# Performance work log

Measured on AMD Instinct MI355X. Metric: run time of the kernel, lower is better.

## Reference

```python
import jax, jax.numpy as jnp
import numpy as np

N = 100000
E = 1600000
NFEAT = 128
NHID1 = 128
NHID2 = 128
NCLASS = 40


def setup_inputs() -> dict:
    key = jax.random.key(0)
    ks = jax.random.split(key, 16)
    x = jax.random.normal(ks[0], (N, NFEAT), dtype=jnp.float32)
    src = jax.random.randint(ks[1], (E,), 0, N, dtype=jnp.int32)
    dst = jax.random.randint(ks[2], (E,), 0, N, dtype=jnp.int32)
    s = 0.05
    params = {
        # SAGE layer 1: self branch and neighbor branch
        'w1s': jax.random.normal(ks[3], (NFEAT, NHID1), dtype=jnp.float32) * s,
        'b1s': jnp.zeros((NHID1,), dtype=jnp.float32),
        'w1n': jax.random.normal(ks[4], (NFEAT, NHID1), dtype=jnp.float32) * s,
        'b1n': jnp.zeros((NHID1,), dtype=jnp.float32),
        # SAGE layer 2 (input dim 2*NHID1)
        'w2s': jax.random.normal(ks[5], (2 * NHID1, NHID2), dtype=jnp.float32) * s,
        'b2s': jnp.zeros((NHID2,), dtype=jnp.float32),
        'w2n': jax.random.normal(ks[6], (2 * NHID1, NHID2), dtype=jnp.float32) * s,
        'b2n': jnp.zeros((NHID2,), dtype=jnp.float32),
        # final linear head (input dim 2*NHID2)
        'wfc': jax.random.normal(ks[7], (2 * NHID2, NCLASS), dtype=jnp.float32) * s,
        'bfc': jnp.zeros((NCLASS,), dtype=jnp.float32),
    }
    return {'x': x, 'src': src, 'dst': dst, **params}


def _neigh_mean(h, src, dst, n_nodes):
    # mean aggregation == spmm(row-normalized adj, h), via segment sum over edges
    msg = jax.ops.segment_sum(h[src], dst, num_segments=n_nodes)  # [N, d]
    cnt = jax.ops.segment_sum(jnp.ones((src.shape[0],), h.dtype), dst, num_segments=n_nodes)
    return msg / jnp.maximum(cnt, 1.0)[:, None]


def _sage_layer(h, src, dst, ws, bs, wn, bn):
    neigh = _neigh_mean(h, src, dst, h.shape[0])
    return jnp.concatenate([h @ ws + bs, neigh @ wn + bn], axis=1)


def _l2_normalize(h, eps=1e-12):
    nrm = jnp.sqrt(jnp.sum(h * h, axis=1, keepdims=True))
    return h / jnp.maximum(nrm, eps)


def reference(x, src, dst, w1s, b1s, w1n, b1n, w2s, b2s, w2n, b2n, wfc, bfc):
    h = jax.nn.relu(_sage_layer(x, src, dst, w1s, b1s, w1n, b1n))  # [N, 2*NHID1]
    h = _l2_normalize(h)
    # dropout is identity in eval mode
    h = jax.nn.relu(_sage_layer(h, src, dst, w2s, b2s, w2n, b2n))  # [N, 2*NHID2]
    h = _l2_normalize(h)
    return h @ wfc + bfc  # [N, NCLASS]
```

## Files before the change

kernel.cpp:

```cpp
#include <hip/hip_runtime.h>
#include <hip/hip_bf16.h>


#define N_NODES 100000
#define N_EDGES 1600000
#define NBUCK   196
#define BCAP    12288
#define PB_CAP  14336
#define CHUNK   4096
#define PREP_BLKS 432
#define GEMM1_BLKS 782

typedef unsigned short u16;
typedef unsigned int u32;
typedef __bf16 bf16x8 __attribute__((ext_vector_type(8)));
typedef float  f32x4  __attribute__((ext_vector_type(4)));

__device__ __forceinline__ u16 f2b(float f) {
  unsigned x = __builtin_bit_cast(unsigned, f);
  unsigned r = x + 0x7fffu + ((x >> 16) & 1u);
  return (u16)(r >> 16);
}
__device__ __forceinline__ bf16x8 ldfrag(const u16* p) {
  uint4 u = *reinterpret_cast<const uint4*>(p);
  return __builtin_bit_cast(bf16x8, u);
}
__device__ __forceinline__ void unpack8(uint4 u, float* f) {
  f[0] = __builtin_bit_cast(float, u.x << 16);
  f[1] = __builtin_bit_cast(float, u.x & 0xffff0000u);
  f[2] = __builtin_bit_cast(float, u.y << 16);
  f[3] = __builtin_bit_cast(float, u.y & 0xffff0000u);
  f[4] = __builtin_bit_cast(float, u.z << 16);
  f[5] = __builtin_bit_cast(float, u.z & 0xffff0000u);
  f[6] = __builtin_bit_cast(float, u.w << 16);
  f[7] = __builtin_bit_cast(float, u.w & 0xffff0000u);
}
__device__ __forceinline__ uint4 pack8(const float* f) {
  uint4 u;
  u.x = (u32)f2b(f[0]) | ((u32)f2b(f[1]) << 16);
  u.y = (u32)f2b(f[2]) | ((u32)f2b(f[3]) << 16);
  u.z = (u32)f2b(f[4]) | ((u32)f2b(f[5]) << 16);
  u.w = (u32)f2b(f[6]) | ((u32)f2b(f[7]) << 16);
  return u;
}

__device__ __forceinline__ int wave_incl_scan(int x, int lane) {
#pragma unroll
  for (int d = 1; d < 64; d <<= 1) {
    int n = __shfl_up(x, d, 64);
    if (lane >= d) x += n;
  }
  return x;
}

__device__ void prep_body(int bid, const float* __restrict__ w1s,
                          const float* __restrict__ w1n,
                          const float* __restrict__ w2s,
                          const float* __restrict__ w2n,
                          const float* __restrict__ wfc, u16* __restrict__ WT1,
                          u16* __restrict__ WT2, u16* __restrict__ WFCT) {
  int i = bid * 256 + threadIdx.x;
  if (i < 32768) {
    int c = i >> 7, k = i & 127;
    float v = (c < 128) ? w1s[k * 128 + c] : w1n[k * 128 + (c - 128)];
    WT1[c * 128 + k] = f2b(v);
  } else if (i < 32768 + 65536) {
    int j = i - 32768;
    int c = j >> 8, k = j & 255;
    float v = (c < 128) ? w2s[k * 128 + c] : w2n[k * 128 + (c - 128)];
    WT2[c * 256 + k] = f2b(v);
  } else {
    int j = i - 98304;
    int c = j >> 8, k = j & 255;
    float v = (c < 40) ? wfc[k * 40 + c] : 0.f;
    WFCT[c * 256 + k] = f2b(v);
  }
}

__global__ __launch_bounds__(256) void prep_bucket_kernel(
    const float* __restrict__ w1s, const float* __restrict__ w1n,
    const float* __restrict__ w2s, const float* __restrict__ w2n,
    const float* __restrict__ wfc, u16* __restrict__ WT1,
    u16* __restrict__ WT2, u16* __restrict__ WFCT,
    const int* __restrict__ src, const int* __restrict__ dst,
    int* __restrict__ cntg, u32* __restrict__ pairBuf) {
  if (blockIdx.x < PREP_BLKS) {
    prep_body(blockIdx.x, w1s, w1n, w2s, w2n, wfc, WT1, WT2, WFCT);
    return;
  }
  __shared__ unsigned hist[NBUCK];
  __shared__ unsigned gbase[NBUCK];
  __shared__ int sws[4];
  __shared__ u32 stage[CHUNK];
  __shared__ int tgt[CHUNK];
  const int tid = threadIdx.x, lane = tid & 63, wid = tid >> 6;
  const int e0 = (blockIdx.x - PREP_BLKS) * CHUNK;

  for (int i = tid; i < NBUCK; i += 256) hist[i] = 0u;
  __syncthreads();

  u32 myW[16];
  int myR[16], myB[16];
#pragma unroll
  for (int k = 0; k < 16; ++k) {
    int e = e0 + k * 256 + tid;
    if (e < N_EDGES) {
      unsigned d = (unsigned)dst[e];
      myW[k] = ((d & 511u) << 17) | (unsigned)src[e];
      myB[k] = (int)(d >> 9);
      myR[k] = (int)atomicAdd(&hist[myB[k]], 1u);
    } else {
      myB[k] = -1;
    }
  }
  __syncthreads();

  int cnt = (tid < NBUCK) ? (int)hist[tid] : 0;
  int inc = wave_incl_scan(cnt, lane);
  if (lane == 63) sws[wid] = inc;
  __syncthreads();
  if (wid == 0) {
    int s = (lane < 4) ? sws[lane] : 0;
    s = wave_incl_scan(s, lane);
    if (lane < 4) sws[lane] = s;
  }
  __syncthreads();
  int excl = (wid ? sws[wid - 1] : 0) + inc - cnt;
  int gofs = 0;
  if (tid < NBUCK && cnt > 0) gofs = tid * BCAP + atomicAdd(&cntg[tid], cnt);
  __syncthreads();
  if (tid < NBUCK) {
    hist[tid] = (unsigned)excl;
    gbase[tid] = (unsigned)gofs;
  }
  __syncthreads();

#pragma unroll
  for (int k = 0; k < 16; ++k) {
    if (myB[k] >= 0) {
      int slot = (int)hist[myB[k]] + myR[k];
      stage[slot] = myW[k];
      tgt[slot] = (int)gbase[myB[k]] + myR[k];
    }
  }
  __syncthreads();
  int nvalid = N_EDGES - e0;
  if (nvalid > CHUNK) nvalid = CHUNK;
  for (int i = tid; i < nvalid; i += 256) pairBuf[tgt[i]] = stage[i];
}

__device__ void csr_body(char* smem, int b, const u32* __restrict__ pairBuf,
                         const int* __restrict__ cntg, int* __restrict__ rowptr,
                         int* __restrict__ degA, int* __restrict__ csr) {
  int* lcnt = (int*)smem;
  int* lofs = lcnt + 512;
  int* sws = lofs + 512;
  int* cstage = sws + 8;
  const int tid = threadIdx.x;
  const int lane = tid & 63, wid = tid >> 6;
  int nb = cntg[b];
  if (nb > BCAP) nb = BCAP;
  const u32* pp = pairBuf + (size_t)b * BCAP;

  lcnt[tid] = 0;
  __syncthreads();
  for (int i = tid; i < nb; i += 512) atomicAdd(&lcnt[(pp[i] >> 17) & 511], 1);
  __syncthreads();
  int dg = lcnt[tid];
  int pd = (dg + 15) & ~15;
  int inc = wave_incl_scan(pd, lane);
  if (lane == 63) sws[wid] = inc;
  __syncthreads();
  if (wid == 0) {
    int s = (lane < 8) ? sws[lane] : 0;
    s = wave_incl_scan(s, lane);
    if (lane < 8) sws[lane] = s;
  }
  __syncthreads();
  int excl = (wid ? sws[wid - 1] : 0) + inc - pd;
  int ptot = sws[7];
  int node = b * 512 + tid;
  if (node < N_NODES) {
    rowptr[node] = b * PB_CAP + excl;
    degA[node] = dg;
  }
  lofs[tid] = excl;
  __syncthreads();
  for (int i = tid; i < nb; i += 512) {
    u32 pr = pp[i];
    int pos = atomicAdd(&lofs[(pr >> 17) & 511], 1);
    if (pos < PB_CAP) cstage[pos] = (int)(pr & 0x1FFFFu);
  }
  __syncthreads();
  for (int k = excl + dg; k < excl + pd; ++k)
    if (k < PB_CAP) cstage[k] = N_NODES;
  __syncthreads();
  if (ptot > PB_CAP) ptot = PB_CAP;
  for (int i = tid; i < ptot; i += 512) csr[b * PB_CAP + i] = cstage[i];
}

__device__ void gemm1_body(char* smem, int bid, const float* __restrict__ A,
                           const u16* __restrict__ WT, u16* __restrict__ Cs,
                           u16* __restrict__ Cn) {
  char* lbc = smem;
  const int tid = threadIdx.x;
  for (int i = tid; i < 4096; i += 512) {
    uint4 v = *reinterpret_cast<const uint4*>(WT + i * 8);
    int byte = i * 16;
    int swz = byte ^ (((byte >> 8) & 7) << 4);
    *reinterpret_cast<uint4*>(lbc + swz) = v;
  }

  const int w = tid >> 6, lane = tid & 63;
  const int lrow = lane & 15, lk = lane >> 4;
  const int xr = (lrow & 7) << 4;
  const int rbase = bid * 128 + w * 16;

  bf16x8 af[4];
  {
    int r = rbase + lrow;
    if (r >= N_NODES) r = N_NODES - 1;
    const float* ap = A + (size_t)r * 128 + lk * 8;
#pragma unroll
    for (int ks = 0; ks < 4; ++ks) {
      float4 f0 = *reinterpret_cast<const float4*>(ap + ks * 32);
      float4 f1 = *reinterpret_cast<const float4*>(ap + ks * 32 + 4);
      float f[8] = {f0.x, f0.y, f0.z, f0.w, f1.x, f1.y, f1.z, f1.w};
      af[ks] = __builtin_bit_cast(bf16x8, pack8(f));
    }
  }
  __syncthreads();

  f32x4 acc[16];
#pragma unroll
  for (int ct = 0; ct < 16; ++ct) acc[ct] = f32x4{0.f, 0.f, 0.f, 0.f};
#pragma unroll
  for (int ks = 0; ks < 4; ++ks) {
#pragma unroll
    for (int ct = 0; ct < 16; ++ct) {
      int byte = (ct * 16 + lrow) * 256 + ks * 64 + lk * 16;
      bf16x8 b = __builtin_bit_cast(
          bf16x8, *reinterpret_cast<const uint4*>(lbc + (byte ^ xr)));
      acc[ct] = __builtin_amdgcn_mfma_f32_16x16x32_bf16(af[ks], b, acc[ct], 0, 0, 0);
    }
  }
#pragma unroll
  for (int j = 0; j < 4; ++j) {
    int r = rbase + lk * 4 + j;
    if (r < N_NODES) {
      u16* cs = Cs + (size_t)r * 128 + lrow;
      u16* cn = Cn + (size_t)r * 128 + lrow;
#pragma unroll
      for (int ct = 0; ct < 8; ++ct) cs[ct * 16] = f2b(acc[ct][j]);
#pragma unroll
      for (int ct = 0; ct < 8; ++ct) cn[ct * 16] = f2b(acc[8 + ct][j]);
    }
  }
}

__global__ __launch_bounds__(512) void csr_gemm1_kernel(
    const u32* __restrict__ pairBuf, const int* __restrict__ cntg,
    int* __restrict__ rowptr, int* __restrict__ degA, int* __restrict__ csr,
    const float* __restrict__ A, const u16* __restrict__ WT,
    u16* __restrict__ Cs, u16* __restrict__ Cn) {
  extern __shared__ char smem[];
  if (blockIdx.x < NBUCK) {
    csr_body(smem, blockIdx.x, pairBuf, cntg, rowptr, degA, csr);
  } else {
    gemm1_body(smem, blockIdx.x - NBUCK, A, WT, Cs, Cn);
  }
}

__device__ __forceinline__ void agg_node(
    const u16* __restrict__ Xs, const u16* __restrict__ Xn,
    const int* __restrict__ rowptr, const int* __restrict__ degA,
    const int* __restrict__ csr, const float* __restrict__ bs,
    const float* __restrict__ bn, int node, int g, int lc,
    float* sf, float* nf) {
  int beg = rowptr[node], dg = degA[node];
  int cnt = (dg + 15) & ~15;
  float acc[8] = {0.f, 0.f, 0.f, 0.f, 0.f, 0.f, 0.f, 0.f};
  const u16* colbase = Xn + lc * 8;
  const int* cp = csr + beg;
  for (int j = 0; j < cnt; j += 16) {
    int s0 = cp[j + g];
    int s1 = cp[j + 4 + g];
    int s2 = cp[j + 8 + g];
    int s3 = cp[j + 12 + g];
    uint4 u0 = *reinterpret_cast<const uint4*>(colbase + (size_t)s0 * 128);
    uint4 u1 = *reinterpret_cast<const uint4*>(colbase + (size_t)s1 * 128);
    uint4 u2 = *reinterpret_cast<const uint4*>(colbase + (size_t)s2 * 128);
    uint4 u3 = *reinterpret_cast<const uint4*>(colbase + (size_t)s3 * 128);
    float f0[8], f1[8], f2[8], f3[8];
    unpack8(u0, f0);
    unpack8(u1, f1);
    unpack8(u2, f2);
    unpack8(u3, f3);
#pragma unroll
    for (int i = 0; i < 8; ++i) acc[i] += (f0[i] + f1[i]) + (f2[i] + f3[i]);
  }
#pragma unroll
  for (int i = 0; i < 8; ++i) {
    acc[i] += __shfl_xor(acc[i], 32, 64);
    acc[i] += __shfl_xor(acc[i], 16, 64);
  }
  float inv = 1.f / (float)(dg > 0 ? dg : 1);
  uint4 sv4 = *reinterpret_cast<const uint4*>(Xs + (size_t)node * 128 + lc * 8);
  unpack8(sv4, sf);
  float4 b0 = *reinterpret_cast<const float4*>(bs + lc * 8);
  float4 b1 = *reinterpret_cast<const float4*>(bs + lc * 8 + 4);
  float4 c0 = *reinterpret_cast<const float4*>(bn + lc * 8);
  float4 c1 = *reinterpret_cast<const float4*>(bn + lc * 8 + 4);
  float bsv[8] = {b0.x, b0.y, b0.z, b0.w, b1.x, b1.y, b1.z, b1.w};
  float bnv[8] = {c0.x, c0.y, c0.z, c0.w, c1.x, c1.y, c1.z, c1.w};
  float ss = 0.f;
#pragma unroll
  for (int i = 0; i < 8; ++i) {
    sf[i] = fmaxf(sf[i] + bsv[i], 0.f);
    nf[i] = fmaxf(acc[i] * inv + bnv[i], 0.f);
    ss += sf[i] * sf[i] + nf[i] * nf[i];
  }
  ss += __shfl_xor(ss, 1, 64);
  ss += __shfl_xor(ss, 2, 64);
  ss += __shfl_xor(ss, 4, 64);
  ss += __shfl_xor(ss, 8, 64);
  float sc = 1.f / fmaxf(sqrtf(ss), 1e-12f);
#pragma unroll
  for (int i = 0; i < 8; ++i) {
    sf[i] *= sc;
    nf[i] *= sc;
  }
}

__global__ __launch_bounds__(256) void agg_epi_kernel(
    const u16* __restrict__ Xs, const u16* __restrict__ Xn,
    const int* __restrict__ rowptr, const int* __restrict__ degA,
    const int* __restrict__ csr, const float* __restrict__ bs,
    const float* __restrict__ bn, u16* __restrict__ H) {
  const int lane = threadIdx.x & 63;
  const int g = lane >> 4, lc = lane & 15;
  const int wave0 = blockIdx.x * 4 + (threadIdx.x >> 6);
  const int stride = gridDim.x * 4;
  for (int node = wave0; node < N_NODES; node += stride) {
    float sf[8], nf[8];
    agg_node(Xs, Xn, rowptr, degA, csr, bs, bn, node, g, lc, sf, nf);
    if (g == 0) {
      *reinterpret_cast<uint4*>(H + (size_t)node * 256 + lc * 8) = pack8(sf);
    } else if (g == 1) {
      *reinterpret_cast<uint4*>(H + (size_t)node * 256 + 128 + lc * 8) = pack8(nf);
    }
  }
}

__global__ __launch_bounds__(512) void gemm2_kernel(
    const u16* __restrict__ A, const u16* __restrict__ WT,
    u16* __restrict__ Cs, u16* __restrict__ Cn) {
  __shared__ u16 lb[128 * 256];
  char* lbc = reinterpret_cast<char*>(lb);
  const int tid = threadIdx.x;
  const int w = tid >> 6, lane = tid & 63;
  const int lrow = lane & 15, lk = lane >> 4;
  const int xr = (lrow & 7) << 4;
  const int rbase = blockIdx.x * 128 + w * 16;

  bf16x8 af[8];
  {
    int r = rbase + lrow;
    if (r >= N_NODES) r = N_NODES - 1;
    const u16* ap = A + (size_t)r * 256 + lk * 8;
#pragma unroll
    for (int ks = 0; ks < 8; ++ks) af[ks] = ldfrag(ap + ks * 32);
  }

#pragma unroll
  for (int half = 0; half < 2; ++half) {
    const u16* Wsrc = WT + (size_t)half * 128 * 256;
    for (int i = tid; i < 4096; i += 512) {
      uint4 v = *reinterpret_cast<const uint4*>(Wsrc + i * 8);
      int byte = i * 16;
      int swz = byte ^ (((byte >> 9) & 7) << 4);
      *reinterpret_cast<uint4*>(lbc + swz) = v;
    }
    __syncthreads();

    f32x4 acc[8];
#pragma unroll
    for (int ct = 0; ct < 8; ++ct) acc[ct] = f32x4{0.f, 0.f, 0.f, 0.f};
#pragma unroll
    for (int ks = 0; ks < 8; ++ks) {
#pragma unroll
      for (int ct = 0; ct < 8; ++ct) {
        int byte = (ct * 16 + lrow) * 512 + ks * 64 + lk * 16;
        bf16x8 b = __builtin_bit_cast(
            bf16x8, *reinterpret_cast<const uint4*>(lbc + (byte ^ xr)));
        acc[ct] = __builtin_amdgcn_mfma_f32_16x16x32_bf16(af[ks], b, acc[ct], 0, 0, 0);
      }
    }
    u16* __restrict__ Cout = half ? Cn : Cs;
#pragma unroll
    for (int j = 0; j < 4; ++j) {
      int r = rbase + lk * 4 + j;
      if (r < N_NODES) {
        u16* cp = Cout + (size_t)r * 128 + lrow;
#pragma unroll
        for (int ct = 0; ct < 8; ++ct) cp[ct * 16] = f2b(acc[ct][j]);
      }
    }
    __syncthreads();
  }
}

__global__ __launch_bounds__(256) void fc_kernel(const u16* __restrict__ H2,
                                                 const u16* __restrict__ WFCT,
                                                 const float* __restrict__ bfc,
                                                 float* __restrict__ Out) {
  __shared__ u16 lb[48 * 256];
  char* lbc = reinterpret_cast<char*>(lb);
  const int tid = threadIdx.x;
#pragma unroll
  for (int i = tid; i < 48 * 256 / 8; i += 256) {
    uint4 v = *reinterpret_cast<const uint4*>(WFCT + i * 8);
    int byte = i * 16;
    int swz = byte ^ (((byte >> 9) & 7) << 4);
    *reinterpret_cast<uint4*>(lbc + swz) = v;
  }
  __syncthreads();
  const int w = tid >> 6, lane = tid & 63;
  const int lrow = lane & 15, lk = lane >> 4;
  const int xr = (lrow & 7) << 4;
  const int rbase = blockIdx.x * 64 + w * 16;

  bf16x8 af[8];
  {
    int r = rbase + lrow;
    if (r >= N_NODES) r = N_NODES - 1;
    const u16* ap = H2 + (size_t)r * 256 + lk * 8;
#pragma unroll
    for (int ks = 0; ks < 8; ++ks) af[ks] = ldfrag(ap + ks * 32);
  }
  f32x4 acc[3];
#pragma unroll
  for (int ct = 0; ct < 3; ++ct) acc[ct] = f32x4{0.f, 0.f, 0.f, 0.f};
#pragma unroll
  for (int ks = 0; ks < 8; ++ks) {
#pragma unroll
    for (int ct = 0; ct < 3; ++ct) {
      int byte = (ct * 16 + lrow) * 512 + ks * 64 + lk * 16;
      bf16x8 b = __builtin_bit_cast(
          bf16x8, *reinterpret_cast<const uint4*>(lbc + (byte ^ xr)));
      acc[ct] = __builtin_amdgcn_mfma_f32_16x16x32_bf16(af[ks], b, acc[ct], 0, 0, 0);
    }
  }
#pragma unroll
  for (int j = 0; j < 4; ++j) {
    int r = rbase + lk * 4 + j;
    if (r < N_NODES) {
#pragma unroll
      for (int ct = 0; ct < 3; ++ct) {
        int col = ct * 16 + lrow;
        if (col < 40) Out[(size_t)r * 40 + col] = acc[ct][j] + bfc[col];
      }
    }
  }
}

extern "C" void kernel_launch(void* const* d_in, const int* in_sizes, int n_in,
                              void* d_out, int out_size, void* d_ws, size_t ws_size,
                              hipStream_t stream) {
  const float* x = (const float*)d_in[0];
  const int* src = (const int*)d_in[1];
  const int* dst = (const int*)d_in[2];
  const float* w1s = (const float*)d_in[3];
  const float* b1s = (const float*)d_in[4];
  const float* w1n = (const float*)d_in[5];
  const float* b1n = (const float*)d_in[6];
  const float* w2s = (const float*)d_in[7];
  const float* b2s = (const float*)d_in[8];
  const float* w2n = (const float*)d_in[9];
  const float* b2n = (const float*)d_in[10];
  const float* wfc = (const float*)d_in[11];
  const float* bfc = (const float*)d_in[12];
  float* out = (float*)d_out;

  char* p = (char*)d_ws;
  auto alloc = [&](size_t bytes) {
    char* r = p;
    p += (bytes + 255) & ~(size_t)255;
    return r;
  };
  u16* XWs = (u16*)alloc((size_t)N_NODES * 128 * 2);
  u16* XWn = (u16*)alloc(((size_t)N_NODES + 1) * 128 * 2);
  u16* h1 = (u16*)alloc((size_t)N_NODES * 256 * 2);
  u16* WT1 = (u16*)alloc(32768 * 2);
  u16* WT2 = (u16*)alloc(65536 * 2);
  u16* WFCT = (u16*)alloc(12288 * 2);
  u32* pairBuf = (u32*)alloc((size_t)NBUCK * BCAP * 4);
  int* cntg = (int*)alloc(NBUCK * 4);
  int* rowptr = (int*)alloc((size_t)N_NODES * 4);
  int* degA = (int*)alloc((size_t)N_NODES * 4);
  int* csr = (int*)alloc((size_t)NBUCK * PB_CAP * 4);
  u16* h2 = h1;

  hipMemsetAsync(cntg, 0, NBUCK * 4, stream);
  hipMemsetAsync(XWn + (size_t)N_NODES * 128, 0, 256, stream);

  prep_bucket_kernel<<<PREP_BLKS + 391, 256, 0, stream>>>(
      w1s, w1n, w2s, w2n, wfc, WT1, WT2, WFCT, src, dst, cntg, pairBuf);
  csr_gemm1_kernel<<<NBUCK + GEMM1_BLKS, 512, 65536, stream>>>(
      pairBuf, cntg, rowptr, degA, csr, x, WT1, XWs, XWn);
  agg_epi_kernel<<<2048, 256, 0, stream>>>(XWs, XWn, rowptr, degA, csr, b1s, b1n, h1);
  gemm2_kernel<<<GEMM1_BLKS, 512, 0, stream>>>(h1, WT2, XWs, XWn);
  agg_epi_kernel<<<2048, 256, 0, stream>>>(XWs, XWn, rowptr, degA, csr, b2s, b2n, h2);
  fc_kernel<<<1563, 256, 0, stream>>>(h2, WFCT, bfc, out);
}
```

Before: 372.8 us.

## Store neighbor-branch projections in FP8 to halve gather traffic

The neighbor-branch projected features (XWn) are now written as FP8 instead of bf16, so each gathered row is 128 bytes instead of 256. The aggregation loop reads 8-byte fragments, converts them with the hardware FP8 unpack instructions, and pads CSR rows to 8 instead of 16 entries. The aggregation kernel also drops the grid-stride loop in favour of one wave per node with a larger grid. The trade is lower precision in the neighbor mean, which may break tolerance, in exchange for less random-gather bandwidth.

Measured after the change: 330.3 us. -11.4%, faster.

```diff
diff --git a/kernel.cpp b/kernel.cpp
--- a/kernel.cpp
+++ b/kernel.cpp
@@ -12,14 +12,20 @@
 #define GEMM1_BLKS 782
 
 typedef unsigned short u16;
+typedef unsigned char u8;
 typedef unsigned int u32;
 typedef __bf16 bf16x8 __attribute__((ext_vector_type(8)));
 typedef float  f32x4  __attribute__((ext_vector_type(4)));
+typedef float  f32x2  __attribute__((ext_vector_type(2)));
 
 __device__ __forceinline__ u16 f2b(float f) {
   unsigned x = __builtin_bit_cast(unsigned, f);
   unsigned r = x + 0x7fffu + ((x >> 16) & 1u);
   return (u16)(r >> 16);
+}
+__device__ __forceinline__ u8 f2fp8(float v) {
+  int p = __builtin_amdgcn_cvt_pk_fp8_f32(v, v, 0, false);
+  return (u8)(p & 0xff);
 }
 __device__ __forceinline__ bf16x8 ldfrag(const u16* p) {
   uint4 u = *reinterpret_cast<const uint4*>(p);
@@ -42,6 +48,16 @@
   u.z = (u32)f2b(f[4]) | ((u32)f2b(f[5]) << 16);
   u.w = (u32)f2b(f[6]) | ((u32)f2b(f[7]) << 16);
   return u;
+}
+__device__ __forceinline__ void addfp8(uint2 a, float* acc) {
+  f32x2 p0 = __builtin_amdgcn_cvt_pk_f32_fp8((int)a.x, false);
+  f32x2 p1 = __builtin_amdgcn_cvt_pk_f32_fp8((int)a.x, true);
+  f32x2 p2 = __builtin_amdgcn_cvt_pk_f32_fp8((int)a.y, false);
+  f32x2 p3 = __builtin_amdgcn_cvt_pk_f32_fp8((int)a.y, true);
+  acc[0] += p0.x; acc[1] += p0.y;
+  acc[2] += p1.x; acc[3] += p1.y;
+  acc[4] += p2.x; acc[5] += p2.y;
+  acc[6] += p3.x; acc[7] += p3.y;
 }
 
 __device__ __forceinline__ int wave_incl_scan(int x, int lane) {
@@ -167,7 +183,7 @@
   for (int i = tid; i < nb; i += 512) atomicAdd(&lcnt[(pp[i] >> 17) & 511], 1);
   __syncthreads();
   int dg = lcnt[tid];
-  int pd = (dg + 15) & ~15;
+  int pd = (dg + 7) & ~7;
   int inc = wave_incl_scan(pd, lane);
   if (lane == 63) sws[wid] = inc;
   __syncthreads();
@@ -201,7 +217,7 @@
 
 __device__ void gemm1_body(char* smem, int bid, const float* __restrict__ A,
                            const u16* __restrict__ WT, u16* __restrict__ Cs,
-                           u16* __restrict__ Cn) {
+                           u8* __restrict__ Cn8) {
   char* lbc = smem;
   const int tid = threadIdx.x;
   for (int i = tid; i < 4096; i += 512) {
@@ -249,11 +265,11 @@
     int r = rbase + lk * 4 + j;
     if (r < N_NODES) {
       u16* cs = Cs + (size_t)r * 128 + lrow;
-      u16* cn = Cn + (size_t)r * 128 + lrow;
+      u8* cn = Cn8 + (size_t)r * 128 + lrow;
 #pragma unroll
       for (int ct = 0; ct < 8; ++ct) cs[ct * 16] = f2b(acc[ct][j]);
 #pragma unroll
-      for (int ct = 0; ct < 8; ++ct) cn[ct * 16] = f2b(acc[8 + ct][j]);
+      for (int ct = 0; ct < 8; ++ct) cn[ct * 16] = f2fp8(acc[8 + ct][j]);
     }
   }
 }
@@ -262,42 +278,33 @@
     const u32* __restrict__ pairBuf, const int* __restrict__ cntg,
     int* __restrict__ rowptr, int* __restrict__ degA, int* __restrict__ csr,
     const float* __restrict__ A, const u16* __restrict__ WT,
-    u16* __restrict__ Cs, u16* __restrict__ Cn) {
+    u16* __restrict__ Cs, u8* __restrict__ Cn8) {
   extern __shared__ char smem[];
   if (blockIdx.x < NBUCK) {
     csr_body(smem, blockIdx.x, pairBuf, cntg, rowptr, degA, csr);
   } else {
-    gemm1_body(smem, blockIdx.x - NBUCK, A, WT, Cs, Cn);
+    gemm1_body(smem, blockIdx.x - NBUCK, A, WT, Cs, Cn8);
   }
 }
 
 __device__ __forceinline__ void agg_node(
-    const u16* __restrict__ Xs, const u16* __restrict__ Xn,
+    const u16* __restrict__ Xs, const u8* __restrict__ Xn8,
     const int* __restrict__ rowptr, const int* __restrict__ degA,
     const int* __restrict__ csr, const float* __restrict__ bs,
     const float* __restrict__ bn, int node, int g, int lc,
     float* sf, float* nf) {
   int beg = rowptr[node], dg = degA[node];
-  int cnt = (dg + 15) & ~15;
+  int cnt = (dg + 7) & ~7;
   float acc[8] = {0.f, 0.f, 0.f, 0.f, 0.f, 0.f, 0.f, 0.f};
-  const u16* colbase = Xn + lc * 8;
+  const u8* colbase = Xn8 + lc * 8;
   const int* cp = csr + beg;
-  for (int j = 0; j < cnt; j += 16) {
+  for (int j = 0; j < cnt; j += 8) {
     int s0 = cp[j + g];
     int s1 = cp[j + 4 + g];
-    int s2 = cp[j + 8 + g];
-    int s3 = cp[j + 12 + g];
-    uint4 u0 = *reinterpret_cast<const uint4*>(colbase + (size_t)s0 * 128);
-    uint4 u1 = *reinterpret_cast<const uint4*>(colbase + (size_t)s1 * 128);
-    uint4 u2 = *reinterpret_cast<const uint4*>(colbase + (size_t)s2 * 128);
-    uint4 u3 = *reinterpret_cast<const uint4*>(colbase + (size_t)s3 * 128);
-    float f0[8], f1[8], f2[8], f3[8];
-    unpack8(u0, f0);
-    unpack8(u1, f1);
-    unpack8(u2, f2);
-    unpack8(u3, f3);
-#pragma unroll
-    for (int i = 0; i < 8; ++i) acc[i] += (f0[i] + f1[i]) + (f2[i] + f3[i]);
+    uint2 a = *reinterpret_cast<const uint2*>(colbase + (size_t)s0 * 128);
+    uint2 b = *reinterpret_cast<const uint2*>(colbase + (size_t)s1 * 128);
+    addfp8(a, acc);
+    addfp8(b, acc);
   }
 #pragma unroll
   for (int i = 0; i < 8; ++i) {
@@ -333,28 +340,26 @@
 }
 
 __global__ __launch_bounds__(256) void agg_epi_kernel(
-    const u16* __restrict__ Xs, const u16* __restrict__ Xn,
+    const u16* __restrict__ Xs, const u8* __restrict__ Xn8,
     const int* __restrict__ rowptr, const int* __restrict__ degA,
     const int* __restrict__ csr, const float* __restrict__ bs,
     const float* __restrict__ bn, u16* __restrict__ H) {
-  const int lane = threadIdx.x & 63;
+  int node = (int)((blockIdx.x * 256 + threadIdx.x) >> 6);
+  int lane = threadIdx.x & 63;
+  if (node >= N_NODES) return;
   const int g = lane >> 4, lc = lane & 15;
-  const int wave0 = blockIdx.x * 4 + (threadIdx.x >> 6);
-  const int stride = gridDim.x * 4;
-  for (int node = wave0; node < N_NODES; node += stride) {
-    float sf[8], nf[8];
-    agg_node(Xs, Xn, rowptr, degA, csr, bs, bn, node, g, lc, sf, nf);
-    if (g == 0) {
-      *reinterpret_cast<uint4*>(H + (size_t)node * 256 + lc * 8) = pack8(sf);
-    } else if (g == 1) {
-      *reinterpret_cast<uint4*>(H + (size_t)node * 256 + 128 + lc * 8) = pack8(nf);
-    }
+  float sf[8], nf[8];
+  agg_node(Xs, Xn8, rowptr, degA, csr, bs, bn, node, g, lc, sf, nf);
+  if (g == 0) {
+    *reinterpret_cast<uint4*>(H + (size_t)node * 256 + lc * 8) = pack8(sf);
+  } else if (g == 1) {
+    *reinterpret_cast<uint4*>(H + (size_t)node * 256 + 128 + lc * 8) = pack8(nf);
   }
 }
 
 __global__ __launch_bounds__(512) void gemm2_kernel(
     const u16* __restrict__ A, const u16* __restrict__ WT,
-    u16* __restrict__ Cs, u16* __restrict__ Cn) {
+    u16* __restrict__ Cs, u8* __restrict__ Cn8) {
   __shared__ u16 lb[128 * 256];
   char* lbc = reinterpret_cast<char*>(lb);
   const int tid = threadIdx.x;
@@ -396,14 +401,19 @@
         acc[ct] = __builtin_amdgcn_mfma_f32_16x16x32_bf16(af[ks], b, acc[ct], 0, 0, 0);
       }
     }
-    u16* __restrict__ Cout = half ? Cn : Cs;
 #pragma unroll
     for (int j = 0; j < 4; ++j) {
       int r = rbase + lk * 4 + j;
       if (r < N_NODES) {
-        u16* cp = Cout + (size_t)r * 128 + lrow;
-#pragma unroll
-        for (int ct = 0; ct < 8; ++ct) cp[ct * 16] = f2b(acc[ct][j]);
+        if (half == 0) {
+          u16* cp = Cs + (size_t)r * 128 + lrow;
+#pragma unroll
+          for (int ct = 0; ct < 8; ++ct) cp[ct * 16] = f2b(acc[ct][j]);
+        } else {
+          u8* cp = Cn8 + (size_t)r * 128 + lrow;
+#pragma unroll
+          for (int ct = 0; ct < 8; ++ct) cp[ct * 16] = f2fp8(acc[ct][j]);
+        }
       }
     }
     __syncthreads();
@@ -489,7 +499,7 @@
     return r;
   };
   u16* XWs = (u16*)alloc((size_t)N_NODES * 128 * 2);
-  u16* XWn = (u16*)alloc(((size_t)N_NODES + 1) * 128 * 2);
+  u8* XWn8 = (u8*)alloc(((size_t)N_NODES + 1) * 128);
   u16* h1 = (u16*)alloc((size_t)N_NODES * 256 * 2);
   u16* WT1 = (u16*)alloc(32768 * 2);
   u16* WT2 = (u16*)alloc(65536 * 2);
@@ -502,14 +512,14 @@
   u16* h2 = h1;
 
   hipMemsetAsync(cntg, 0, NBUCK * 4, stream);
-  hipMemsetAsync(XWn + (size_t)N_NODES * 128, 0, 256, stream);
+  hipMemsetAsync(XWn8 + (size_t)N_NODES * 128, 0, 128, stream);
 
   prep_bucket_kernel<<<PREP_BLKS + 391, 256, 0, stream>>>(
       w1s, w1n, w2s, w2n, wfc, WT1, WT2, WFCT, src, dst, cntg, pairBuf);
   csr_gemm1_kernel<<<NBUCK + GEMM1_BLKS, 512, 65536, stream>>>(
-      pairBuf, cntg, rowptr, degA, csr, x, WT1, XWs, XWn);
-  agg_epi_kernel<<<2048, 256, 0, stream>>>(XWs, XWn, rowptr, degA, csr, b1s, b1n, h1);
-  gemm2_kernel<<<GEMM1_BLKS, 512, 0, stream>>>(h1, WT2, XWs, XWn);
-  agg_epi_kernel<<<2048, 256, 0, stream>>>(XWs, XWn, rowptr, degA, csr, b2s, b2n, h2);
+      pairBuf, cntg, rowptr, degA, csr, x, WT1, XWs, XWn8);
+  agg_epi_kernel<<<25000, 256, 0, stream>>>(XWs, XWn8, rowptr, degA, csr, b1s, b1n, h1);
+  gemm2_kernel<<<GEMM1_BLKS, 512, 0, stream>>>(h1, WT2, XWs, XWn8);
+  agg_epi_kernel<<<25000, 256, 0, stream>>>(XWs, XWn8, rowptr, degA, csr, b2s, b2n, h2);
   fc_kernel<<<1563, 256, 0, stream>>>(h2, WFCT, bfc, out);
 }
```
